# Performance work log

Hardware: AMD Instinct MI355X
Metric: run time of the kernel (lower is better)

## Reference

```python
import jax, jax.numpy as jnp
import numpy as np

NUM_CLASSES = 22
MARGIN = 0.01  # margin of the hinge on squared point distance


def quat_to_rotmat(q):
    # q: [..., 4] unit quaternion in (w, x, y, z) order -> [..., 3, 3]
    w, x, y, z = q[..., 0], q[..., 1], q[..., 2], q[..., 3]
    return jnp.stack([
        jnp.stack([1 - 2 * (y * y + z * z), 2 * (x * y - z * w), 2 * (x * z + y * w)], -1),
        jnp.stack([2 * (x * y + z * w), 1 - 2 * (x * x + z * z), 2 * (y * z - x * w)], -1),
        jnp.stack([2 * (x * z - y * w), 2 * (y * z + x * w), 1 - 2 * (x * x + y * y)], -1),
    ], -2)


def setup_inputs() -> dict:
    key = jax.random.key(0)
    B, C, P = 128, NUM_CLASSES, 1024
    ks = jax.random.split(key, 5)
    qp = jax.random.normal(ks[0], (B, C, 4), dtype=jnp.float32)
    qp = qp / jnp.linalg.norm(qp, axis=-1, keepdims=True)
    qg = jax.random.normal(ks[1], (B, C, 4), dtype=jnp.float32)
    qg = qg / jnp.linalg.norm(qg, axis=-1, keepdims=True)
    cls = jax.random.randint(ks[2], (B,), 1, C)  # skip background class 0
    poses_weight = jnp.repeat(jax.nn.one_hot(cls, C, dtype=jnp.float32), 4, axis=1)  # [B, 4C]
    points = 0.05 * jax.random.normal(ks[3], (C, P, 3), dtype=jnp.float32)  # object models (~meters)
    symmetry = (jax.random.uniform(ks[4], (C,)) < 0.5).astype(jnp.float32)
    return {
        'poses_pred': qp.reshape(B, 4 * C),
        'poses_target': qg.reshape(B, 4 * C),
        'poses_weight': poses_weight,
        'points': points,
        'symmetry': symmetry,
    }


def reference(poses_pred, poses_target, poses_weight, points, symmetry):
    B = poses_pred.shape[0]
    P = points.shape[1]
    # class selection: first class i with weight[n, 4i] > 0 (as in the CUDA kernel)
    w = poses_weight.reshape(B, NUM_CLASSES, 4)[:, :, 0]
    valid = jnp.any(w > 0, axis=1)
    cls = jnp.argmax(w > 0, axis=1)

    rows = jnp.arange(B)
    q_pred = poses_pred.reshape(B, NUM_CLASSES, 4)[rows, cls]   # [B,4]
    q_gt = poses_target.reshape(B, NUM_CLASSES, 4)[rows, cls]   # [B,4]
    pts = points[cls]                                           # [B,P,3] gather per class
    sym = symmetry[cls] > 0                                     # [B]

    Rp = quat_to_rotmat(q_pred)
    Rg = quat_to_rotmat(q_gt)
    xp = jnp.einsum('bij,bpj->bpi', Rp, pts)  # predicted-pose rotated points [B,P,3]
    xg = jnp.einsum('bij,bpj->bpi', Rg, pts)  # target-pose rotated points   [B,P,3]

    # ADD: matched squared distance
    d_diag = jnp.sum((xp - xg) ** 2, axis=-1)  # [B,P]
    # ADD-S: nearest-neighbor squared distance via ||a||^2 + ||b||^2 - 2 a.b
    d2 = (jnp.sum(xp * xp, -1)[:, :, None] + jnp.sum(xg * xg, -1)[:, None, :]
          - 2.0 * jnp.einsum('bpc,bqc->bpq', xp, xg))  # [B,P,P]
    d_sym = jnp.min(jnp.maximum(d2, 0.0), axis=2)       # [B,P]

    d = jnp.where(sym[:, None], d_sym, d_diag)
    per_point = 0.5 * jnp.maximum(d - MARGIN, 0.0)       # margin-clamped
    per_point = per_point * valid[:, None].astype(per_point.dtype)
    return jnp.sum(per_point) / (B * P)
```

## Files before the change

kernel.cpp:

```cpp
#include <hip/hip_runtime.h>
#include <math.h>

#define NUM_CLASSES 22
#define MARGIN 0.01f
#define PTS 1024
#define BLOCK 256
#define PPT 4

__device__ __forceinline__ void quat_to_rot(const float* __restrict__ q, float R[9]) {
    float w = q[0], x = q[1], y = q[2], z = q[3];
    R[0] = 1.f - 2.f * (y * y + z * z);
    R[1] = 2.f * (x * y - z * w);
    R[2] = 2.f * (x * z + y * w);
    R[3] = 2.f * (x * y + z * w);
    R[4] = 1.f - 2.f * (x * x + z * z);
    R[5] = 2.f * (y * z - x * w);
    R[6] = 2.f * (x * z - y * w);
    R[7] = 2.f * (y * z + x * w);
    R[8] = 1.f - 2.f * (x * x + y * y);
}

__device__ __forceinline__ int find_class(const float* wrow) {
    for (int c = 0; c < NUM_CLASSES; ++c)
        if (wrow[4 * c] > 0.f) return c;
    return -1;
}

__global__ __launch_bounds__(BLOCK) void adl_min_kernel(
    const float* __restrict__ poses_pred,
    const float* __restrict__ poses_target,
    const float* __restrict__ poses_weight,
    const float* __restrict__ points,
    const float* __restrict__ symmetry,
    float* __restrict__ out,
    float* __restrict__ ws,
    int S)
{
    __shared__ float4 s_h[PTS];

    if (blockIdx.x == 0 && threadIdx.x == 0) out[0] = 0.f;

    const int b = blockIdx.x / S;
    const int s = blockIdx.x - b * S;
    const int tid = threadIdx.x;

    const int cls = find_class(poses_weight + (size_t)b * 4 * NUM_CLASSES);
    if (cls < 0) return;
    if (!(symmetry[cls] > 0.f)) return;

    float Rp[9], Rg[9];
    quat_to_rot(poses_pred + ((size_t)b * NUM_CLASSES + cls) * 4, Rp);
    quat_to_rot(poses_target + ((size_t)b * NUM_CLASSES + cls) * 4, Rg);
    const float* pts = points + (size_t)cls * PTS * 3;

    const int QS = PTS / S;
    const int qbase = s * QS;

    for (int q = tid; q < QS; q += BLOCK) {
        float px = pts[3 * (qbase + q) + 0];
        float py = pts[3 * (qbase + q) + 1];
        float pz = pts[3 * (qbase + q) + 2];
        float gx = Rg[0] * px + Rg[1] * py + Rg[2] * pz;
        float gy = Rg[3] * px + Rg[4] * py + Rg[5] * pz;
        float gz = Rg[6] * px + Rg[7] * py + Rg[8] * pz;
        s_h[q] = make_float4(-2.f * gx, -2.f * gy, -2.f * gz,
                             gx * gx + gy * gy + gz * gz);
    }
    __syncthreads();

    float ax[PPT], ay[PPT], az[PPT], m[PPT];
    #pragma unroll
    for (int j = 0; j < PPT; ++j) {
        const int p = tid + j * BLOCK;
        float px = pts[3 * p + 0];
        float py = pts[3 * p + 1];
        float pz = pts[3 * p + 2];
        ax[j] = Rp[0] * px + Rp[1] * py + Rp[2] * pz;
        ay[j] = Rp[3] * px + Rp[4] * py + Rp[5] * pz;
        az[j] = Rp[6] * px + Rp[7] * py + Rp[8] * pz;
        m[j] = INFINITY;
    }

    #pragma unroll 4
    for (int q = 0; q < QS; ++q) {
        float4 h = s_h[q];
        #pragma unroll
        for (int j = 0; j < PPT; ++j) {
            float t = fmaf(az[j], h.z, h.w);
            t = fmaf(ay[j], h.y, t);
            t = fmaf(ax[j], h.x, t);
            m[j] = fminf(m[j], t);
        }
    }

    #pragma unroll
    for (int j = 0; j < PPT; ++j) {
        const int p = tid + j * BLOCK;
        ws[((size_t)b * PTS + p) * S + s] = m[j];
    }
}

__global__ __launch_bounds__(BLOCK) void adl_finish_kernel(
    const float* __restrict__ poses_pred,
    const float* __restrict__ poses_target,
    const float* __restrict__ poses_weight,
    const float* __restrict__ points,
    const float* __restrict__ symmetry,
    float* __restrict__ out,
    const float* __restrict__ ws,
    int S, float inv_scale)
{
    __shared__ float s_part[BLOCK / 64];
    const int b = blockIdx.x;
    const int tid = threadIdx.x;

    const int cls = find_class(poses_weight + (size_t)b * 4 * NUM_CLASSES);
    if (cls < 0) return;

    float Rp[9], Rg[9];
    quat_to_rot(poses_pred + ((size_t)b * NUM_CLASSES + cls) * 4, Rp);
    quat_to_rot(poses_target + ((size_t)b * NUM_CLASSES + cls) * 4, Rg);
    const bool sym = symmetry[cls] > 0.f;
    const float* pts = points + (size_t)cls * PTS * 3;

    float sum = 0.f;
    #pragma unroll
    for (int j = 0; j < PPT; ++j) {
        const int p = tid + j * BLOCK;
        float px = pts[3 * p + 0];
        float py = pts[3 * p + 1];
        float pz = pts[3 * p + 2];
        float axv = Rp[0] * px + Rp[1] * py + Rp[2] * pz;
        float ayv = Rp[3] * px + Rp[4] * py + Rp[5] * pz;
        float azv = Rp[6] * px + Rp[7] * py + Rp[8] * pz;
        float d;
        if (sym) {
            float mv = INFINITY;
            const float* w = ws + ((size_t)b * PTS + p) * S;
            for (int s = 0; s < S; ++s) mv = fminf(mv, w[s]);
            float na = axv * axv + ayv * ayv + azv * azv;
            d = fmaxf(na + mv, 0.f);
        } else {
            float gx = Rg[0] * px + Rg[1] * py + Rg[2] * pz;
            float gy = Rg[3] * px + Rg[4] * py + Rg[5] * pz;
            float gz = Rg[6] * px + Rg[7] * py + Rg[8] * pz;
            float dx = axv - gx, dy = ayv - gy, dz = azv - gz;
            d = dx * dx + dy * dy + dz * dz;
        }
        sum += 0.5f * fmaxf(d - MARGIN, 0.f);
    }

    #pragma unroll
    for (int off = 32; off > 0; off >>= 1)
        sum += __shfl_down(sum, off, 64);
    const int wave = tid >> 6;
    if ((tid & 63) == 0) s_part[wave] = sum;
    __syncthreads();
    if (tid == 0) {
        float s = 0.f;
        #pragma unroll
        for (int w = 0; w < BLOCK / 64; ++w) s += s_part[w];
        atomicAdd(out, s * inv_scale);
    }
}

extern "C" void kernel_launch(void* const* d_in, const int* in_sizes, int n_in,
                              void* d_out, int out_size, void* d_ws, size_t ws_size,
                              hipStream_t stream) {
    const float* poses_pred   = (const float*)d_in[0];
    const float* poses_target = (const float*)d_in[1];
    const float* poses_weight = (const float*)d_in[2];
    const float* points       = (const float*)d_in[3];
    const float* symmetry     = (const float*)d_in[4];
    float* out = (float*)d_out;
    float* ws  = (float*)d_ws;

    const int B = in_sizes[0] / (4 * NUM_CLASSES);
    const float inv_scale = 1.0f / ((float)B * (float)PTS);

    int S = 8;
    while (S > 1 && (size_t)B * PTS * S * sizeof(float) > ws_size) S >>= 1;

    adl_min_kernel<<<B * S, BLOCK, 0, stream>>>(
        poses_pred, poses_target, poses_weight, points, symmetry, out, ws, S);
    adl_finish_kernel<<<B, BLOCK, 0, stream>>>(
        poses_pred, poses_target, poses_weight, points, symmetry, out, ws, S, inv_scale);
}
```

Measured before the change: 81.91 us.

## Fuse min and finish kernels, split query points across lane groups

Merges the two-kernel ADD-S pipeline into one kernel. Each block now handles a slice of 128 prediction points, and groups of 8 lanes split the 1024 target points, combining their partial minima with xor shuffles. This drops the workspace round trip and the second launch, and the output is zeroed with a memset. The cost is that every block recomputes all 1024 rotated target points into shared memory, giving 8 blocks per batch with redundant setup, and the sums are now combined with more atomics.

```diff
diff --git a/kernel.cpp b/kernel.cpp
--- a/kernel.cpp
+++ b/kernel.cpp
@@ -5,19 +5,25 @@
 #define MARGIN 0.01f
 #define PTS 1024
 #define BLOCK 256
+#define R 8
 #define PPT 4
+#define PGRP (BLOCK / R)
+#define PBLK (PGRP * PPT)
+#define SBLK (PTS / PBLK)
+#define QT (PTS / R)
+#define HSTRIDE (QT + 1)
 
-__device__ __forceinline__ void quat_to_rot(const float* __restrict__ q, float R[9]) {
+__device__ __forceinline__ void quat_to_rot(const float* __restrict__ q, float R_[9]) {
     float w = q[0], x = q[1], y = q[2], z = q[3];
-    R[0] = 1.f - 2.f * (y * y + z * z);
-    R[1] = 2.f * (x * y - z * w);
-    R[2] = 2.f * (x * z + y * w);
-    R[3] = 2.f * (x * y + z * w);
-    R[4] = 1.f - 2.f * (x * x + z * z);
-    R[5] = 2.f * (y * z - x * w);
-    R[6] = 2.f * (x * z - y * w);
-    R[7] = 2.f * (y * z + x * w);
-    R[8] = 1.f - 2.f * (x * x + y * y);
+    R_[0] = 1.f - 2.f * (y * y + z * z);
+    R_[1] = 2.f * (x * y - z * w);
+    R_[2] = 2.f * (x * z + y * w);
+    R_[3] = 2.f * (x * y + z * w);
+    R_[4] = 1.f - 2.f * (x * x + z * z);
+    R_[5] = 2.f * (y * z - x * w);
+    R_[6] = 2.f * (x * z - y * w);
+    R_[7] = 2.f * (y * z + x * w);
+    R_[8] = 1.f - 2.f * (x * x + y * y);
 }
 
 __device__ __forceinline__ int find_class(const float* wrow) {
@@ -26,92 +32,20 @@
     return -1;
 }
 
-__global__ __launch_bounds__(BLOCK) void adl_min_kernel(
+__global__ __launch_bounds__(BLOCK) void adl_kernel(
     const float* __restrict__ poses_pred,
     const float* __restrict__ poses_target,
     const float* __restrict__ poses_weight,
     const float* __restrict__ points,
     const float* __restrict__ symmetry,
     float* __restrict__ out,
-    float* __restrict__ ws,
-    int S)
+    float inv_scale)
 {
-    __shared__ float4 s_h[PTS];
+    __shared__ float4 s_h[R * HSTRIDE];
+    __shared__ float s_part[BLOCK / 64];
 
-    if (blockIdx.x == 0 && threadIdx.x == 0) out[0] = 0.f;
-
-    const int b = blockIdx.x / S;
-    const int s = blockIdx.x - b * S;
-    const int tid = threadIdx.x;
-
-    const int cls = find_class(poses_weight + (size_t)b * 4 * NUM_CLASSES);
-    if (cls < 0) return;
-    if (!(symmetry[cls] > 0.f)) return;
-
-    float Rp[9], Rg[9];
-    quat_to_rot(poses_pred + ((size_t)b * NUM_CLASSES + cls) * 4, Rp);
-    quat_to_rot(poses_target + ((size_t)b * NUM_CLASSES + cls) * 4, Rg);
-    const float* pts = points + (size_t)cls * PTS * 3;
-
-    const int QS = PTS / S;
-    const int qbase = s * QS;
-
-    for (int q = tid; q < QS; q += BLOCK) {
-        float px = pts[3 * (qbase + q) + 0];
-        float py = pts[3 * (qbase + q) + 1];
-        float pz = pts[3 * (qbase + q) + 2];
-        float gx = Rg[0] * px + Rg[1] * py + Rg[2] * pz;
-        float gy = Rg[3] * px + Rg[4] * py + Rg[5] * pz;
-        float gz = Rg[6] * px + Rg[7] * py + Rg[8] * pz;
-        s_h[q] = make_float4(-2.f * gx, -2.f * gy, -2.f * gz,
-                             gx * gx + gy * gy + gz * gz);
-    }
-    __syncthreads();
-
-    float ax[PPT], ay[PPT], az[PPT], m[PPT];
-    #pragma unroll
-    for (int j = 0; j < PPT; ++j) {
-        const int p = tid + j * BLOCK;
-        float px = pts[3 * p + 0];
-        float py = pts[3 * p + 1];
-        float pz = pts[3 * p + 2];
-        ax[j] = Rp[0] * px + Rp[1] * py + Rp[2] * pz;
-        ay[j] = Rp[3] * px + Rp[4] * py + Rp[5] * pz;
-        az[j] = Rp[6] * px + Rp[7] * py + Rp[8] * pz;
-        m[j] = INFINITY;
-    }
-
-    #pragma unroll 4
-    for (int q = 0; q < QS; ++q) {
-        float4 h = s_h[q];
-        #pragma unroll
-        for (int j = 0; j < PPT; ++j) {
-            float t = fmaf(az[j], h.z, h.w);
-            t = fmaf(ay[j], h.y, t);
-            t = fmaf(ax[j], h.x, t);
-            m[j] = fminf(m[j], t);
-        }
-    }
-
-    #pragma unroll
-    for (int j = 0; j < PPT; ++j) {
-        const int p = tid + j * BLOCK;
-        ws[((size_t)b * PTS + p) * S + s] = m[j];
-    }
-}
-
-__global__ __launch_bounds__(BLOCK) void adl_finish_kernel(
-    const float* __restrict__ poses_pred,
-    const float* __restrict__ poses_target,
-    const float* __restrict__ poses_weight,
-    const float* __restrict__ points,
-    const float* __restrict__ symmetry,
-    float* __restrict__ out,
-    const float* __restrict__ ws,
-    int S, float inv_scale)
-{
-    __shared__ float s_part[BLOCK / 64];
-    const int b = blockIdx.x;
+    const int b = blockIdx.x / SBLK;
+    const int s = blockIdx.x - b * SBLK;
     const int tid = threadIdx.x;
 
     const int cls = find_class(poses_weight + (size_t)b * 4 * NUM_CLASSES);
@@ -124,30 +58,82 @@
     const float* pts = points + (size_t)cls * PTS * 3;
 
     float sum = 0.f;
-    #pragma unroll
-    for (int j = 0; j < PPT; ++j) {
-        const int p = tid + j * BLOCK;
-        float px = pts[3 * p + 0];
-        float py = pts[3 * p + 1];
-        float pz = pts[3 * p + 2];
-        float axv = Rp[0] * px + Rp[1] * py + Rp[2] * pz;
-        float ayv = Rp[3] * px + Rp[4] * py + Rp[5] * pz;
-        float azv = Rp[6] * px + Rp[7] * py + Rp[8] * pz;
-        float d;
-        if (sym) {
-            float mv = INFINITY;
-            const float* w = ws + ((size_t)b * PTS + p) * S;
-            for (int s = 0; s < S; ++s) mv = fminf(mv, w[s]);
-            float na = axv * axv + ayv * ayv + azv * azv;
-            d = fmaxf(na + mv, 0.f);
-        } else {
+
+    if (sym) {
+        #pragma unroll
+        for (int k = 0; k < PTS / BLOCK; ++k) {
+            const int Q = tid + k * BLOCK;
+            float px = pts[3 * Q + 0];
+            float py = pts[3 * Q + 1];
+            float pz = pts[3 * Q + 2];
+            float gx = Rg[0] * px + Rg[1] * py + Rg[2] * pz;
+            float gy = Rg[3] * px + Rg[4] * py + Rg[5] * pz;
+            float gz = Rg[6] * px + Rg[7] * py + Rg[8] * pz;
+            s_h[(Q >> 7) * HSTRIDE + (Q & (QT - 1))] =
+                make_float4(-2.f * gx, -2.f * gy, -2.f * gz,
+                            gx * gx + gy * gy + gz * gz);
+        }
+        __syncthreads();
+
+        const int qq = tid & (R - 1);
+        const int pg = tid >> 3;
+
+        float ax[PPT], ay[PPT], az[PPT], na[PPT], m[PPT];
+        #pragma unroll
+        for (int j = 0; j < PPT; ++j) {
+            const int p = s * PBLK + pg + j * PGRP;
+            float px = pts[3 * p + 0];
+            float py = pts[3 * p + 1];
+            float pz = pts[3 * p + 2];
+            ax[j] = Rp[0] * px + Rp[1] * py + Rp[2] * pz;
+            ay[j] = Rp[3] * px + Rp[4] * py + Rp[5] * pz;
+            az[j] = Rp[6] * px + Rp[7] * py + Rp[8] * pz;
+            na[j] = ax[j] * ax[j] + ay[j] * ay[j] + az[j] * az[j];
+            m[j] = INFINITY;
+        }
+
+        const float4* __restrict__ hq = s_h + qq * HSTRIDE;
+        #pragma unroll 4
+        for (int q = 0; q < QT; ++q) {
+            float4 h = hq[q];
+            #pragma unroll
+            for (int j = 0; j < PPT; ++j) {
+                float t = fmaf(az[j], h.z, h.w);
+                t = fmaf(ay[j], h.y, t);
+                t = fmaf(ax[j], h.x, t);
+                m[j] = fminf(m[j], t);
+            }
+        }
+
+        #pragma unroll
+        for (int j = 0; j < PPT; ++j) {
+            #pragma unroll
+            for (int d = 1; d < R; d <<= 1)
+                m[j] = fminf(m[j], __shfl_xor(m[j], d, 64));
+        }
+        if (qq == 0) {
+            #pragma unroll
+            for (int j = 0; j < PPT; ++j) {
+                float dd = fmaxf(na[j] + m[j], 0.f);
+                sum += 0.5f * fmaxf(dd - MARGIN, 0.f);
+            }
+        }
+    } else {
+        if (tid < PBLK) {
+            const int p = s * PBLK + tid;
+            float px = pts[3 * p + 0];
+            float py = pts[3 * p + 1];
+            float pz = pts[3 * p + 2];
+            float axv = Rp[0] * px + Rp[1] * py + Rp[2] * pz;
+            float ayv = Rp[3] * px + Rp[4] * py + Rp[5] * pz;
+            float azv = Rp[6] * px + Rp[7] * py + Rp[8] * pz;
             float gx = Rg[0] * px + Rg[1] * py + Rg[2] * pz;
             float gy = Rg[3] * px + Rg[4] * py + Rg[5] * pz;
             float gz = Rg[6] * px + Rg[7] * py + Rg[8] * pz;
             float dx = axv - gx, dy = ayv - gy, dz = azv - gz;
-            d = dx * dx + dy * dy + dz * dz;
+            float d = dx * dx + dy * dy + dz * dz;
+            sum = 0.5f * fmaxf(d - MARGIN, 0.f);
         }
-        sum += 0.5f * fmaxf(d - MARGIN, 0.f);
     }
 
     #pragma unroll
@@ -157,10 +143,10 @@
     if ((tid & 63) == 0) s_part[wave] = sum;
     __syncthreads();
     if (tid == 0) {
-        float s = 0.f;
+        float total = 0.f;
         #pragma unroll
-        for (int w = 0; w < BLOCK / 64; ++w) s += s_part[w];
-        atomicAdd(out, s * inv_scale);
+        for (int w = 0; w < BLOCK / 64; ++w) total += s_part[w];
+        atomicAdd(out, total * inv_scale);
     }
 }
 
@@ -173,16 +159,11 @@
     const float* points       = (const float*)d_in[3];
     const float* symmetry     = (const float*)d_in[4];
     float* out = (float*)d_out;
-    float* ws  = (float*)d_ws;
 
     const int B = in_sizes[0] / (4 * NUM_CLASSES);
     const float inv_scale = 1.0f / ((float)B * (float)PTS);
 
-    int S = 8;
-    while (S > 1 && (size_t)B * PTS * S * sizeof(float) > ws_size) S >>= 1;
-
-    adl_min_kernel<<<B * S, BLOCK, 0, stream>>>(
-        poses_pred, poses_target, poses_weight, points, symmetry, out, ws, S);
-    adl_finish_kernel<<<B, BLOCK, 0, stream>>>(
-        poses_pred, poses_target, poses_weight, points, symmetry, out, ws, S, inv_scale);
+    hipMemsetAsync(out, 0, sizeof(float), stream);
+    adl_kernel<<<B * SBLK, BLOCK, 0, stream>>>(
+        poses_pred, poses_target, poses_weight, points, symmetry, out, inv_scale);
 }
```

Result: faster. 78.92 us (-3.7%).
